# Optimization experiments

Hardware: AMD Instinct MI355X
Metric: run time of the kernel (lower is better)

Reference implementation:

```python
import jax, jax.numpy as jnp
import numpy as np

EPS = 1.0  # global `epsilon` in the original code
B, C, N, T = 4, 32, 256, 288
NUM_PRED, NUM_LOCAL = 12, 12
PERIOD, SHORT, LONG = 24, 12, 48
EMB = 16
RE_K = 5  # ResidualExtrapolate kernel width (num_input)


def const_extrap(x, p):
    # replicate-pad right by p along time
    return jnp.concatenate([x, jnp.repeat(x[..., -1:], p, axis=-1)], axis=-1)


def seasonal_extrap(x, p):
    # circular-pad right by p along time (p <= t)
    return jnp.concatenate([x, x[..., :p]], axis=-1)


def term_norm(x, L):
    # sliding-window mean/var over last axis, window L, replicate-padded left.
    pad1 = [(0, 0)] * 3 + [(1, 0)]
    cs = jnp.pad(jnp.cumsum(x, axis=-1), pad1)
    cs2 = jnp.pad(jnp.cumsum(x * x, axis=-1), pad1)
    mean = (cs[..., L:] - cs[..., :-L]) / L            # (b,c,n,t-L+1)
    var = (cs2[..., L:] - cs2[..., :-L]) / L - mean ** 2 + 1e-5
    padL = [(0, 0)] * 3 + [(L - 1, 0)]
    mean = jnp.pad(mean, padL, mode='edge')
    var = jnp.pad(var, padL, mode='edge')
    out = (x - mean) / jnp.sqrt(var + EPS)
    return out, mean, jnp.sqrt(var)


def seasonal_norm(x, P):
    b, c, n, t = x.shape
    xp = x.reshape(b, c, n, t // P, P)
    mean = xp.mean(3)                                   # (b,c,n,P) per-phase
    var = (xp ** 2).mean(3) - mean ** 2 + 1e-5
    mean = jnp.tile(mean, (1, 1, 1, t // P))
    var = jnp.tile(var, (1, 1, 1, t // P))
    out = (x - mean) / jnp.sqrt(var + EPS)
    return out, mean, jnp.sqrt(var)


def spatial_norm(x, emb):
    n = emb.shape[0]
    adj = emb @ emb.T - 10.0 * jnp.eye(n, dtype=x.dtype)
    adj = jax.nn.softmax(adj, axis=-1)                  # (n,n)
    mean = jnp.einsum('nm,bcmt->bcnt', adj, x)
    var = jnp.einsum('nm,bcmt->bcnt', adj, x * x) - mean ** 2 + 1e-5
    out = (x - mean) / jnp.sqrt(var + EPS)
    return out, mean, jnp.sqrt(var)


def residual_extrap(x, W, bias):
    # Conv2d(c -> c*num_pred, kernel (1, RE_K)) on last RE_K steps, then cat.
    b, c, n, t = x.shape
    y = jnp.einsum('ock,bcnk->bon', W[:, :, 0, :], x[..., -RE_K:]) + bias[None, :, None]
    proj = y.reshape(b, NUM_PRED, c, n).transpose(0, 2, 3, 1)  # (b,c,n,num_pred)
    return jnp.concatenate([x, proj], axis=-1)


def conv_time(x, W, bias):
    y = jax.lax.conv_general_dilated(x, W, (1, 1), 'VALID',
                                     dimension_numbers=('NCHW', 'OIHW', 'NCHW'))
    return y + bias[None, :, None, None]


def conv1x1(x, W, bias):
    return jnp.einsum('oc,bcnt->bont', W[:, :, 0, 0], x) + bias[None, :, None, None]


def setup_inputs() -> dict:
    key = jax.random.key(0)
    ks = jax.random.split(key, 16)
    f32 = jnp.float32

    def w(k, shape, fan_in):
        return jax.random.normal(k, shape, dtype=f32) / np.sqrt(fan_in)

    inp = {
        'x': jax.random.normal(ks[0], (B, C, N, T), dtype=f32),
        'node_embedding': 0.1 * jax.random.normal(ks[1], (N, EMB), dtype=f32),
        'conv1_w': w(ks[6], (C, 13 * C, 1, NUM_LOCAL), 13 * C * NUM_LOCAL),
        'conv1_b': jnp.zeros((C,), f32),
        'conv2_w': w(ks[7], (C, 13 * C, 1, NUM_LOCAL), 13 * C * NUM_LOCAL),
        'conv2_b': jnp.zeros((C,), f32),
        'skip_w': w(ks[8], (C, C, 1, 1), C),
        'skip_b': jnp.zeros((C,), f32),
        'res_w': w(ks[9], (C, C, 1, 1), C),
        'res_b': jnp.zeros((C,), f32),
    }
    for i in range(4):
        inp[f're{i + 1}_w'] = w(ks[2 + i], (C * NUM_PRED, C, 1, RE_K), C * RE_K)
        inp[f're{i + 1}_b'] = jnp.zeros((C * NUM_PRED,), f32)
    return inp


def reference(x, node_embedding, conv1_w, conv1_b, conv2_w, conv2_b,
              skip_w, skip_b, res_w, res_b,
              re1_w, re1_b, re2_w, re2_b, re3_w, re3_b, re4_w, re4_b):
    xs, aux = [], []

    x_proj = const_extrap(x, NUM_PRED)
    zeros = jnp.zeros_like(x_proj)
    xs.append(x_proj); aux.append(zeros)

    x1, lt_mean, lt_std = term_norm(x, LONG)
    xp = residual_extrap(x1, re1_w, re1_b)
    mp, sp = const_extrap(lt_mean, NUM_PRED), const_extrap(lt_std, NUM_PRED)
    xs += [xp, mp, sp]; aux += [zeros, mp, sp]

    x2, se_mean, se_std = seasonal_norm(x1, PERIOD)
    xp = residual_extrap(x2, re2_w, re2_b)
    mp, sp = seasonal_extrap(se_mean, NUM_PRED), seasonal_extrap(se_std, NUM_PRED)
    xs += [xp, mp, sp]; aux += [zeros, mp, sp]

    x3, st_mean, st_std = term_norm(x2, SHORT)
    xp = residual_extrap(x3, re3_w, re3_b)
    mp, sp = const_extrap(st_mean, NUM_PRED), const_extrap(st_std, NUM_PRED)
    xs += [xp, mp, sp]; aux += [zeros, mp, sp]

    x4, sn_mean, sn_std = spatial_norm(x3, node_embedding)
    xp = residual_extrap(x4, re4_w, re4_b)
    mp, sp = const_extrap(sn_mean, NUM_PRED), const_extrap(sn_std, NUM_PRED)
    xs += [xp, mp, sp]; aux += [zeros, mp, sp]

    pad1 = [(0, 0)] * 3 + [(1, 0)]
    x_cat = jnp.pad(jnp.concatenate(xs, axis=1), pad1)      # (b,13c,n,T+P+1)
    a_cat = jnp.pad(jnp.concatenate(aux, axis=1), pad1)

    g1 = conv_time(x_cat, conv1_w, conv1_b)
    g2 = conv_time(x_cat, conv2_w, conv2_b)
    a1 = conv_time(a_cat, conv1_w, conv1_b)
    a2 = conv_time(a_cat, conv2_w, conv2_b)

    prod = g1 * g2
    x_z = conv1x1(prod[..., :-NUM_PRED], res_w, res_b)
    s = conv1x1(prod[..., -NUM_PRED:], skip_w, skip_b)
    s_aux = conv1x1((a1 * a2)[..., -NUM_PRED:], skip_w, skip_b)
    return (x_z, s_aux, s)
```

## Files before the change

kernel.cpp:

```cpp
#include <hip/hip_runtime.h>

typedef unsigned short u16;
typedef __attribute__((ext_vector_type(8))) short short8v;
typedef __attribute__((ext_vector_type(4))) float f32x4;

#define PSTR 304L
#define OFF_SAUX 9109504L
#define OFF_S    9502720L
#define CHSTR (32L*256L*PSTR)

static __device__ __forceinline__ float bf2f(u16 u) {
  return __uint_as_float(((unsigned int)u) << 16);
}
static __device__ __forceinline__ u16 f2bf(float f) {
  unsigned int i = __float_as_uint(f);
  i += 0x7FFFu + ((i >> 16) & 1u);
  return (u16)(i >> 16);
}

static __device__ __forceinline__ void gload16(const void* g, void* l) {
  __builtin_amdgcn_global_load_lds(
      (const __attribute__((address_space(1))) unsigned int*)g,
      (__attribute__((address_space(3))) unsigned int*)l, 16, 0, 0);
}

static __device__ void adj_body(int row, const float* __restrict__ emb,
                                u16* __restrict__ adjb) {
  const int m = threadIdx.x;
  __shared__ float sred[8];
  float er[16];
#pragma unroll
  for (int e = 0; e < 16; ++e) er[e] = emb[row * 16 + e];
  float d = 0.f;
#pragma unroll
  for (int e = 0; e < 16; ++e) d += er[e] * emb[m * 16 + e];
  if (m == row) d -= 10.f;
  float v = d;
#pragma unroll
  for (int off = 32; off; off >>= 1) v = fmaxf(v, __shfl_xor(v, off, 64));
  const int wid = m >> 6, lane = m & 63;
  if (lane == 0) sred[wid] = v;
  __syncthreads();
  const float mx = fmaxf(fmaxf(sred[0], sred[1]), fmaxf(sred[2], sred[3]));
  const float p = expf(d - mx);
  v = p;
#pragma unroll
  for (int off = 32; off; off >>= 1) v += __shfl_xor(v, off, 64);
  if (lane == 0) sred[4 + wid] = v;
  __syncthreads();
  const float sum = sred[4] + sred[5] + sred[6] + sred[7];
  adjb[row * 256 + m] = f2bf(p / sum);
}

static __device__ void prepw_body(int bid, const float* __restrict__ c1w,
                                  const float* __restrict__ c2w,
                                  u16* __restrict__ wB) {
  const int idx = bid * 256 + threadIdx.x;
  const int kk = idx >> 11;
  const int rem = idx & 2047;
  const int j = rem >> 5, chp = rem & 31;
  const int pslot = chp >> 3, chlo = chp & 7;
  const int sl = pslot ^ ((j >> 1) & 3);
  const int ch = sl * 8 + chlo;
  const int g = kk / 12, k = kk - g * 12;
  const int cin = g * 32 + ch;
  const float* src = (j < 32) ? c1w : c2w;
  const int jj = j & 31;
  wB[idx] = f2bf(src[(jj * 416 + cin) * 12 + k]);
}

static __device__ __forceinline__ void wscan2(float& s1, float& s2, int lane) {
#pragma unroll
  for (int off = 1; off < 64; off <<= 1) {
    float a = __shfl_up(s1, off, 64);
    float b = __shfl_up(s2, off, 64);
    if (lane >= off) { s1 += a; s2 += b; }
  }
}

static __device__ void norm_body(int bid, const float* __restrict__ x,
                                 u16* __restrict__ xcat) {
  const int wid = threadIdx.x >> 6, lane = threadIdx.x & 63;
  const long row = (long)bid * 4 + wid;
  const int b = (int)(row >> 13);
  const int c = (int)((row >> 8) & 31);
  const int n = (int)(row & 255);
  const float* xr = x + row * 288;
  __shared__ float bufA[4][304], bufB[4][304], cs1[4][312], cs2[4][312], sst[4][80];
  float* bA = bufA[wid];
  float* bB = bufB[wid];
  float* p1 = cs1[wid];
  float* p2 = cs2[wid];
  float* psm = sst[wid];
  float* psi = sst[wid] + 24;
  float* psd = sst[wid] + 48;
  const long chb = (long)b * 416 * 256 + n;

  for (int j = 0; j < 5; ++j) { int t = j * 64 + lane; if (t < 288) bA[t] = xr[t]; }

  auto scanbuf = [&](float* src) {
    float ca = 0.f, cb = 0.f;
    if (lane == 0) { p1[0] = 0.f; p2[0] = 0.f; }
    for (int j = 0; j < 5; ++j) {
      int t = j * 64 + lane;
      float v = (t < 288) ? src[t] : 0.f;
      float s1 = v, s2 = v * v;
      wscan2(s1, s2, lane);
      if (t < 288) { p1[t + 1] = ca + s1; p2[t + 1] = cb + s2; }
      ca += __shfl(s1, 63, 64);
      cb += __shfl(s2, 63, 64);
    }
  };

  scanbuf(bA);
  for (int j = 0; j < 5; ++j) {
    int t = j * 64 + lane; if (t >= 288) continue;
    float S, Q;
    if (t >= 47) { S = p1[t + 1] - p1[t - 47]; Q = p2[t + 1] - p2[t - 47]; }
    else         { S = p1[48];                 Q = p2[48]; }
    float m = S * (1.f / 48.f);
    float var = Q * (1.f / 48.f) - m * m + 1e-5f;
    float sd = sqrtf(var);
    float iv = rsqrtf(var + 1.f);
    float xv = bA[t];
    float x1 = (xv - m) * iv;
    bB[t] = x1;
    xcat[(chb + (long)(c)      * 256) * PSTR + 1 + t] = f2bf(xv);
    xcat[(chb + (long)(32 + c) * 256) * PSTR + 1 + t] = f2bf(x1);
    xcat[(chb + (long)(64 + c) * 256) * PSTR + 1 + t] = f2bf(m);
    xcat[(chb + (long)(96 + c) * 256) * PSTR + 1 + t] = f2bf(sd);
  }
  {
    float S = p1[288] - p1[240], Q = p2[288] - p2[240];
    float m = S * (1.f / 48.f);
    float var = Q * (1.f / 48.f) - m * m + 1e-5f;
    float sd = sqrtf(var);
    if (lane < 12) {
      xcat[(chb + (long)(c)      * 256) * PSTR + 289 + lane] = f2bf(bA[287]);
      xcat[(chb + (long)(64 + c) * 256) * PSTR + 289 + lane] = f2bf(m);
      xcat[(chb + (long)(96 + c) * 256) * PSTR + 289 + lane] = f2bf(sd);
    }
    if (lane == 0) {
      xcat[(chb + (long)(c)      * 256) * PSTR] = 0;
      xcat[(chb + (long)(32 + c) * 256) * PSTR] = 0;
      xcat[(chb + (long)(64 + c) * 256) * PSTR] = 0;
      xcat[(chb + (long)(96 + c) * 256) * PSTR] = 0;
    }
  }
  if (lane < 24) {
    float S = 0.f, Q = 0.f;
#pragma unroll
    for (int i2 = 0; i2 < 12; ++i2) { float v = bB[lane + 24 * i2]; S += v; Q += v * v; }
    float m = S * (1.f / 12.f);
    float var = Q * (1.f / 12.f) - m * m + 1e-5f;
    psm[lane] = m; psi[lane] = rsqrtf(var + 1.f); psd[lane] = sqrtf(var);
  }
  for (int j = 0; j < 5; ++j) {
    int t = j * 64 + lane; if (t >= 288) continue;
    int ph = t % 24;
    float m = psm[ph];
    float x2v = (bB[t] - m) * psi[ph];
    bA[t] = x2v;
    xcat[(chb + (long)(128 + c) * 256) * PSTR + 1 + t] = f2bf(x2v);
    xcat[(chb + (long)(160 + c) * 256) * PSTR + 1 + t] = f2bf(m);
    xcat[(chb + (long)(192 + c) * 256) * PSTR + 1 + t] = f2bf(psd[ph]);
  }
  if (lane < 12) {
    xcat[(chb + (long)(160 + c) * 256) * PSTR + 289 + lane] = f2bf(psm[lane]);
    xcat[(chb + (long)(192 + c) * 256) * PSTR + 289 + lane] = f2bf(psd[lane]);
  }
  if (lane == 0) {
    xcat[(chb + (long)(128 + c) * 256) * PSTR] = 0;
    xcat[(chb + (long)(160 + c) * 256) * PSTR] = 0;
    xcat[(chb + (long)(192 + c) * 256) * PSTR] = 0;
  }
  scanbuf(bA);
  for (int j = 0; j < 5; ++j) {
    int t = j * 64 + lane; if (t >= 288) continue;
    float S, Q;
    if (t >= 11) { S = p1[t + 1] - p1[t - 11]; Q = p2[t + 1] - p2[t - 11]; }
    else         { S = p1[12];                 Q = p2[12]; }
    float m = S * (1.f / 12.f);
    float var = Q * (1.f / 12.f) - m * m + 1e-5f;
    float sd = sqrtf(var);
    float iv = rsqrtf(var + 1.f);
    float x3v = (bA[t] - m) * iv;
    xcat[(chb + (long)(224 + c) * 256) * PSTR + 1 + t] = f2bf(x3v);
    xcat[(chb + (long)(256 + c) * 256) * PSTR + 1 + t] = f2bf(m);
    xcat[(chb + (long)(288 + c) * 256) * PSTR + 1 + t] = f2bf(sd);
  }
  {
    float S = p1[288] - p1[276], Q = p2[288] - p2[276];
    float m = S * (1.f / 12.f);
    float var = Q * (1.f / 12.f) - m * m + 1e-5f;
    float sd = sqrtf(var);
    if (lane < 12) {
      xcat[(chb + (long)(256 + c) * 256) * PSTR + 289 + lane] = f2bf(m);
      xcat[(chb + (long)(288 + c) * 256) * PSTR + 289 + lane] = f2bf(sd);
    }
    if (lane == 0) {
      xcat[(chb + (long)(224 + c) * 256) * PSTR] = 0;
      xcat[(chb + (long)(256 + c) * 256) * PSTR] = 0;
      xcat[(chb + (long)(288 + c) * 256) * PSTR] = 0;
    }
  }
}

__global__ __launch_bounds__(256) void k_front(const float* __restrict__ x,
    const float* __restrict__ emb, const float* __restrict__ c1w,
    const float* __restrict__ c2w, u16* __restrict__ xcat,
    u16* __restrict__ adjb, u16* __restrict__ wB) {
  const int bid = blockIdx.x;
  if (bid < 8192)       norm_body(bid, x, xcat);
  else if (bid < 8448)  adj_body(bid - 8192, emb, adjb);
  else                  prepw_body(bid - 8448, c1w, c2w, wB);
}

static __device__ void re_body(long gid, u16* __restrict__ xcat,
                               const float* __restrict__ W,
                               const float* __restrict__ bias, int srcch) {
  const int o = (int)(gid % 384);
  const long bn = gid / 384;
  const int n = (int)(bn & 255);
  const int b = (int)(bn >> 8);
  const float* wr = W + o * 160;
  float acc = bias[o];
  for (int c = 0; c < 32; ++c) {
    const long rb = ((long)(b * 416 + srcch + c) * 256 + n) * PSTR + 284;
#pragma unroll
    for (int k = 0; k < 5; ++k) acc += wr[c * 5 + k] * bf2f(xcat[rb + k]);
  }
  const int cd = o & 31, p = o >> 5;
  xcat[((long)(b * 416 + srcch + cd) * 256 + n) * PSTR + 289 + p] = f2bf(acc);
}

__global__ __launch_bounds__(256) void k_re4(u16* __restrict__ xcat,
                                             const float* __restrict__ W,
                                             const float* __restrict__ bias) {
  re_body((long)blockIdx.x * 256 + threadIdx.x, xcat, W, bias, 320);
}

static __device__ void spatial_body(int sid, u16* __restrict__ xcat,
                                    const u16* __restrict__ adjb) {
  const int gx = sid % 20;
  const int slice = sid / 20;
  const int tcn = gx >> 2, ncb = gx & 3;
  const int b = slice >> 5, c = slice & 31;
  const int t0 = tcn * 64, n0 = ncb * 64;
  const int tid = threadIdx.x;
  const int wid = tid >> 6, lane = tid & 63;
  const int wm = wid >> 1, wn = wid & 1;
  const int l15 = lane & 15, lq = lane >> 4;
  __shared__ __align__(16) u16 BT[2][64 * 40];
  __shared__ __align__(16) u16 BT2[2][64 * 40];
  const f32x4 vz = {0.f, 0.f, 0.f, 0.f};
  f32x4 aM[2][2], aV[2][2];
#pragma unroll
  for (int i = 0; i < 2; ++i)
#pragma unroll
    for (int j = 0; j < 2; ++j) { aM[i][j] = vz; aV[i][j] = vz; }
  const long base7 = (long)(b * 416 + 224 + c) * 256;
  u16 rv[8];
#pragma unroll
  for (int r = 0; r < 8; ++r) {
    int idx = tid + r * 256; int ml = idx >> 6, s = idx & 63;
    rv[r] = xcat[(base7 + ml) * PSTR + 1 + t0 + s];
  }
#pragma unroll
  for (int r = 0; r < 8; ++r) {
    int idx = tid + r * 256; int ml = idx >> 6, s = idx & 63;
    float v = bf2f(rv[r]);
    BT[0][s * 40 + ml] = rv[r];
    BT2[0][s * 40 + ml] = f2bf(v * v);
  }
  __syncthreads();
  int cur = 0;
  for (int kk = 0; kk < 8; ++kk) {
    u16 rn[8];
    if (kk < 7) {
#pragma unroll
      for (int r = 0; r < 8; ++r) {
        int idx = tid + r * 256; int ml = idx >> 6, s = idx & 63;
        rn[r] = xcat[(base7 + (long)((kk + 1) * 32 + ml)) * PSTR + 1 + t0 + s];
      }
    }
    const short8v a0 = *(const short8v*)(adjb + (long)(n0 + wm * 32 + l15) * 256 + kk * 32 + lq * 8);
    const short8v a1 = *(const short8v*)(adjb + (long)(n0 + wm * 32 + 16 + l15) * 256 + kk * 32 + lq * 8);
    const u16* bt = BT[cur];
    const u16* bq = BT2[cur];
    const short8v b0 = *(const short8v*)(bt + (wn * 32 + l15) * 40 + lq * 8);
    const short8v b1 = *(const short8v*)(bt + (wn * 32 + 16 + l15) * 40 + lq * 8);
    const short8v q0 = *(const short8v*)(bq + (wn * 32 + l15) * 40 + lq * 8);
    const short8v q1 = *(const short8v*)(bq + (wn * 32 + 16 + l15) * 40 + lq * 8);
    aM[0][0] = __builtin_amdgcn_mfma_f32_16x16x32_bf16(a0, b0, aM[0][0], 0, 0, 0);
    aM[0][1] = __builtin_amdgcn_mfma_f32_16x16x32_bf16(a0, b1, aM[0][1], 0, 0, 0);
    aM[1][0] = __builtin_amdgcn_mfma_f32_16x16x32_bf16(a1, b0, aM[1][0], 0, 0, 0);
    aM[1][1] = __builtin_amdgcn_mfma_f32_16x16x32_bf16(a1, b1, aM[1][1], 0, 0, 0);
    aV[0][0] = __builtin_amdgcn_mfma_f32_16x16x32_bf16(a0, q0, aV[0][0], 0, 0, 0);
    aV[0][1] = __builtin_amdgcn_mfma_f32_16x16x32_bf16(a0, q1, aV[0][1], 0, 0, 0);
    aV[1][0] = __builtin_amdgcn_mfma_f32_16x16x32_bf16(a1, q0, aV[1][0], 0, 0, 0);
    aV[1][1] = __builtin_amdgcn_mfma_f32_16x16x32_bf16(a1, q1, aV[1][1], 0, 0, 0);
    __syncthreads();
    if (kk < 7) {
#pragma unroll
      for (int r = 0; r < 8; ++r) {
        int idx = tid + r * 256; int ml = idx >> 6, s = idx & 63;
        float v = bf2f(rn[r]);
        BT[cur ^ 1][s * 40 + ml] = rn[r];
        BT2[cur ^ 1][s * 40 + ml] = f2bf(v * v);
      }
    }
    __syncthreads();
    cur ^= 1;
  }
#pragma unroll
  for (int mf = 0; mf < 2; ++mf)
#pragma unroll
    for (int nf = 0; nf < 2; ++nf)
#pragma unroll
      for (int e = 0; e < 4; ++e) {
        const int i = wm * 32 + mf * 16 + lq * 4 + e;
        const int j = wn * 32 + nf * 16 + l15;
        const int nn = n0 + i, tt2 = t0 + j;
        if (tt2 < 288) {
          const float mean = aM[mf][nf][e], ex2 = aV[mf][nf][e];
          const float var = ex2 - mean * mean + 1e-5f;
          const float sd = sqrtf(var);
          const float iv = rsqrtf(var + 1.f);
          const float x3c = bf2f(xcat[(base7 + nn) * PSTR + 1 + tt2]);
          const float x4 = (x3c - mean) * iv;
          const long r10 = ((long)(b * 416 + 320 + c) * 256 + nn) * PSTR;
          const long r11 = ((long)(b * 416 + 352 + c) * 256 + nn) * PSTR;
          const long r12 = ((long)(b * 416 + 384 + c) * 256 + nn) * PSTR;
          xcat[r10 + 1 + tt2] = f2bf(x4);
          xcat[r11 + 1 + tt2] = f2bf(mean);
          xcat[r12 + 1 + tt2] = f2bf(sd);
          if (tt2 == 287) {
            for (int p = 0; p < 12; ++p) {
              xcat[r11 + 289 + p] = f2bf(mean);
              xcat[r12 + 289 + p] = f2bf(sd);
            }
          }
          if (tt2 == 0) { xcat[r10] = 0; xcat[r11] = 0; xcat[r12] = 0; }
        }
      }
}

__global__ __launch_bounds__(256) void k_mid(u16* __restrict__ xcat,
    const u16* __restrict__ adjb,
    const float* __restrict__ w1, const float* __restrict__ b1,
    const float* __restrict__ w2, const float* __restrict__ b2,
    const float* __restrict__ w3, const float* __restrict__ b3) {
  const int bid = blockIdx.x;
  if (bid < 2560) { spatial_body(bid, xcat, adjb); return; }
  const int sub = bid - 2560;
  const int which = sub / 1536;
  const long gid = (long)(sub - which * 1536) * 256 + threadIdx.x;
  if (which == 0)      re_body(gid, xcat, w1, b1, 32);
  else if (which == 1) re_body(gid, xcat, w2, b2, 128);
  else                 re_body(gid, xcat, w3, b3, 224);
}

template<int MT>
static __device__ void convG_body(int t0, int by,
    const u16* __restrict__ xcat, const u16* __restrict__ wB,
    const float* __restrict__ c1b, const float* __restrict__ c2b,
    const float* __restrict__ rsw, const float* __restrict__ rsb,
    const float* __restrict__ skw, const float* __restrict__ skb,
    float* __restrict__ out, unsigned char* smem) {
  const int b = by >> 6;
  const int tid = threadIdx.x;
  const int wid = tid >> 6, lane = tid & 63;
  const int n_abs = (by & 63) * 4 + wid;
  const int l15 = lane & 15, lq = lane >> 4;
  constexpr int NCH = (MT == 2) ? 9 : 5;
  constexpr int TKS = (MT == 2) ? 18 : 10;

  u16* Asm = (u16*)smem;
  u16* Bsm = (u16*)(smem + 46080);

  int sch[NCH], stk[NCH];
  const u16* baseR[NCH];
#pragma unroll
  for (int r = 0; r < NCH; ++r) {
    int cc = r * 64 + lane;
    int s = cc / TKS, tk = cc - s * TKS;
    sch[r] = s; stk[r] = tk;
    baseR[r] = xcat + ((long)(b * 416 + s) * 256 + n_abs) * PSTR + t0 + tk * 8;
  }
  u16* aw = Asm + wid * 5760;

#define AWRITE() { \
    _Pragma("unroll") \
    for (int r = 0; r < NCH; ++r) { \
      u16 pc[8]; *(uint4*)pc = aR[r]; \
      const int pcol = ((((sch[r] >> 3) ^ stk[r]) & 3) << 3) + (sch[r] & 7); \
      _Pragma("unroll") \
      for (int e = 0; e < 8; ++e) aw[(stk[r] * 8 + e) * 40 + pcol] = pc[e]; \
    } }

  uint4 aR[NCH];
#pragma unroll
  for (int r = 0; r < NCH; ++r) aR[r] = *(const uint4*)baseR[r];
  AWRITE();
#pragma unroll
  for (int r = 0; r < NCH; ++r) aR[r] = *(const uint4*)(baseR[r] + CHSTR);
  gload16(wB + 0 * 2048 + wid * 512 + lane * 8, Bsm + 0 + wid * 512);
  gload16(wB + 1 * 2048 + wid * 512 + lane * 8, Bsm + 2048 + wid * 512);
  __syncthreads();

  const f32x4 vz = {0.f, 0.f, 0.f, 0.f};
  f32x4 acc[4 * MT][4];
#pragma unroll
  for (int i = 0; i < 4 * MT; ++i)
#pragma unroll
    for (int j = 0; j < 4; ++j) acc[i][j] = vz;

  const u16* bwl = Bsm + l15 * 32 + ((lq ^ ((l15 >> 1) & 3)) << 3);

  int p = 0;
  for (int g = 0; g < 13; ++g) {
    for (int kp = 0; kp < 6; ++kp) {
      if (p < 77) {
        const long kkn = (long)(p + 1) * 2;
        const int bufn = ((p + 1) & 1) * 4096;
        gload16(wB + kkn * 2048 + wid * 512 + lane * 8, Bsm + bufn + wid * 512);
        gload16(wB + (kkn + 1) * 2048 + wid * 512 + lane * 8, Bsm + bufn + 2048 + wid * 512);
      }
      const int bufc = (p & 1) * 4096;
#pragma unroll
      for (int kh = 0; kh < 2; ++kh) {
        const int K = kp * 2 + kh;
        short8v af[4 * MT], bf[4];
#pragma unroll
        for (int f = 0; f < 4 * MT; ++f) {
          const int tt = K + f * 16 + l15;
          af[f] = *(const short8v*)(aw + tt * 40 + (((lq ^ (tt >> 3)) & 3) << 3));
        }
#pragma unroll
        for (int f = 0; f < 4; ++f)
          bf[f] = *(const short8v*)(bwl + bufc + kh * 2048 + f * 512);
#pragma unroll
        for (int i = 0; i < 4 * MT; ++i)
#pragma unroll
          for (int j = 0; j < 4; ++j)
            acc[i][j] = __builtin_amdgcn_mfma_f32_16x16x32_bf16(af[i], bf[j], acc[i][j], 0, 0, 0);
      }
      __syncthreads();
      ++p;
    }
    if (g < 12) {
      AWRITE();
      if (g < 11) {
#pragma unroll
        for (int r = 0; r < NCH; ++r) aR[r] = *(const uint4*)(baseR[r] + (long)(g + 2) * CHSTR);
      }
    }
  }
#undef AWRITE
  __syncthreads();

#pragma unroll
  for (int pass = 0; pass < MT; ++pass) {
    float* pw = (float*)smem + wid * 2112;
#pragma unroll
    for (int fi = 0; fi < 4; ++fi)
#pragma unroll
      for (int nf = 0; nf < 2; ++nf)
#pragma unroll
        for (int e = 0; e < 4; ++e) {
          const int trow = fi * 16 + lq * 4 + e;
          const int cch = nf * 16 + l15;
          const float g1 = acc[pass * 4 + fi][nf][e] + c1b[cch];
          const float g2 = acc[pass * 4 + fi][nf + 2][e] + c2b[cch];
          pw[trow * 33 + cch] = g1 * g2;
        }
    float pv[32];
    {
      const float* prow = pw + lane * 33;
#pragma unroll
      for (int c = 0; c < 32; ++c) pv[c] = prow[c];
    }
    const int t = t0 + pass * 64 + lane;
    if (t0 + pass * 64 + 63 < 278) {
      for (int o = 0; o < 32; ++o) {
        float s = rsb[o];
        const float* wr = rsw + o * 32;
#pragma unroll
        for (int c = 0; c < 32; ++c) s += wr[c] * pv[c];
        out[((long)(b * 32 + o) * 256 + n_abs) * 278 + t] = s;
      }
    } else {
      const bool isres = t < 278;
      const bool isskip = (t >= 278) && (t < 290);
      for (int o = 0; o < 32; ++o) {
        const float* wr = (isres ? rsw : skw) + o * 32;
        float s = (isres ? rsb : skb)[o];
#pragma unroll
        for (int c = 0; c < 32; ++c) s += wr[c] * pv[c];
        if (isres)       out[((long)(b * 32 + o) * 256 + n_abs) * 278 + t] = s;
        else if (isskip) out[OFF_S + ((long)(b * 32 + o) * 256 + n_abs) * 12 + (t - 278)] = s;
      }
    }
  }
}

__global__ __launch_bounds__(256, 2) void k_convG(
    const u16* __restrict__ xcat, const u16* __restrict__ wB,
    const float* __restrict__ c1b, const float* __restrict__ c2b,
    const float* __restrict__ rsw, const float* __restrict__ rsb,
    const float* __restrict__ skw, const float* __restrict__ skb,
    float* __restrict__ out) {
  __shared__ __align__(16) unsigned char smem[62464];
  if (blockIdx.x < 2)
    convG_body<2>(blockIdx.x * 128, blockIdx.y, xcat, wB, c1b, c2b, rsw, rsb, skw, skb, out, smem);
  else
    convG_body<1>(256, blockIdx.y, xcat, wB, c1b, c2b, rsw, rsb, skw, skb, out, smem);
}

__global__ __launch_bounds__(256) void k_convA(const u16* __restrict__ xcat,
    const u16* __restrict__ wB, const float* __restrict__ c1b,
    const float* __restrict__ c2b, const float* __restrict__ skw,
    const float* __restrict__ skb, float* __restrict__ out) {
  const int tid = threadIdx.x;
  const int wid = tid >> 6, lane = tid & 63;
  const int row = blockIdx.x;
  const int b = row >> 8, n = row & 255;
  const int l15 = lane & 15, lq = lane >> 4;
  __shared__ __align__(16) u16 ATa[4][2][36 * 40];
  __shared__ float apL[4][16 * 68];
  const int gtab[8] = {2, 3, 5, 6, 8, 9, 11, 12};
  const long bnbase = (long)b * 416 * 256 + n;

#pragma unroll
  for (int tau = 0; tau < 2; ++tau) {
    const int g = gtab[wid * 2 + tau];
    u16* at = ATa[wid][tau];
#pragma unroll
    for (int h = 0; h < 2; ++h) {
      const int c = lane + h * 64;
      const int ch = c >> 2, part = c & 3;
      const uint4 v = *(const uint4*)(xcat +
          (bnbase + (long)(g * 32 + ch) * 256) * PSTR + 272 + part * 8);
      u16 pc[8]; *(uint4*)pc = v;
#pragma unroll
      for (int e = 0; e < 8; ++e) at[(part * 8 + e) * 40 + ch] = pc[e];
    }
  }

  const f32x4 vz = {0.f, 0.f, 0.f, 0.f};
  f32x4 acc[4] = {vz, vz, vz, vz};
  const int bsw = (lq ^ ((l15 >> 1) & 3)) << 3;
#pragma unroll
  for (int tau = 0; tau < 2; ++tau) {
    const int g = gtab[wid * 2 + tau];
    const u16* at = ATa[wid][tau];
    for (int k = 0; k < 12; ++k) {
      const short8v af = *(const short8v*)(at + (l15 + k + 6) * 40 + lq * 8);
#pragma unroll
      for (int nf = 0; nf < 4; ++nf) {
        const short8v bf = *(const short8v*)(wB + (long)(g * 12 + k) * 2048 + (nf * 16 + l15) * 32 + bsw);
        acc[nf] = __builtin_amdgcn_mfma_f32_16x16x32_bf16(af, bf, acc[nf], 0, 0, 0);
      }
    }
  }
  float* ap = apL[wid];
#pragma unroll
  for (int nf = 0; nf < 4; ++nf)
#pragma unroll
    for (int e = 0; e < 4; ++e)
      ap[(lq * 4 + e) * 68 + nf * 16 + l15] = acc[nf][e];
  __syncthreads();
  for (int idx = tid; idx < 1024; idx += 256) {
    const int m = idx >> 6, j = idx & 63;
    apL[0][m * 68 + j] = apL[0][m * 68 + j] + apL[1][m * 68 + j]
                       + apL[2][m * 68 + j] + apL[3][m * 68 + j];
  }
  __syncthreads();
  for (int task = tid; task < 384; task += 256) {
    const int o = task & 31, tt = task >> 5;
    float s = skb[o];
#pragma unroll
    for (int c2 = 0; c2 < 32; ++c2)
      s += skw[o * 32 + c2] * (apL[0][tt * 68 + c2] + c1b[c2])
                            * (apL[0][tt * 68 + 32 + c2] + c2b[c2]);
    out[OFF_SAUX + ((long)(b * 32 + o) * 256 + n) * 12 + tt] = s;
  }
}

extern "C" void kernel_launch(void* const* d_in, const int* in_sizes, int n_in,
                              void* d_out, int out_size, void* d_ws, size_t ws_size,
                              hipStream_t stream) {
  const float* x   = (const float*)d_in[0];
  const float* emb = (const float*)d_in[1];
  const float* c1w = (const float*)d_in[2];
  const float* c1b = (const float*)d_in[3];
  const float* c2w = (const float*)d_in[4];
  const float* c2b = (const float*)d_in[5];
  const float* skw = (const float*)d_in[6];
  const float* skb = (const float*)d_in[7];
  const float* rsw = (const float*)d_in[8];
  const float* rsb = (const float*)d_in[9];
  float* out = (float*)d_out;

  u16* xcat = (u16*)d_ws;
  u16* wB   = xcat + (4L * 416 * 256 * 304 + 2048);
  u16* adjb = wB + 156L * 2048;

  k_front<<<dim3(9696), dim3(256), 0, stream>>>(x, emb, c1w, c2w, xcat, adjb, wB);
  k_mid<<<dim3(7168), dim3(256), 0, stream>>>(xcat, adjb,
      (const float*)d_in[10], (const float*)d_in[11],
      (const float*)d_in[12], (const float*)d_in[13],
      (const float*)d_in[14], (const float*)d_in[15]);
  k_re4<<<dim3(1536), dim3(256), 0, stream>>>(xcat, (const float*)d_in[16], (const float*)d_in[17]);
  k_convG<<<dim3(3, 256), dim3(256), 0, stream>>>(xcat, wB, c1b, c2b, rsw, rsb, skw, skb, out);
  k_convA<<<dim3(1024), dim3(256), 0, stream>>>(xcat, wB, c1b, c2b, skw, skb, out);
}
```

Measured before the change: 604.9 us.

## Load conv weights directly from global memory instead of LDS double-buffering

```diff
diff --git a/kernel.cpp b/kernel.cpp
--- a/kernel.cpp
+++ b/kernel.cpp
@@ -16,12 +16,6 @@
   unsigned int i = __float_as_uint(f);
   i += 0x7FFFu + ((i >> 16) & 1u);
   return (u16)(i >> 16);
-}
-
-static __device__ __forceinline__ void gload16(const void* g, void* l) {
-  __builtin_amdgcn_global_load_lds(
-      (const __attribute__((address_space(1))) unsigned int*)g,
-      (__attribute__((address_space(3))) unsigned int*)l, 16, 0, 0);
 }
 
 static __device__ void adj_body(int row, const float* __restrict__ emb,
@@ -377,7 +371,6 @@
   constexpr int TKS = (MT == 2) ? 18 : 10;
 
   u16* Asm = (u16*)smem;
-  u16* Bsm = (u16*)(smem + 46080);
 
   int sch[NCH], stk[NCH];
   const u16* baseR[NCH];
@@ -403,11 +396,6 @@
 #pragma unroll
   for (int r = 0; r < NCH; ++r) aR[r] = *(const uint4*)baseR[r];
   AWRITE();
-#pragma unroll
-  for (int r = 0; r < NCH; ++r) aR[r] = *(const uint4*)(baseR[r] + CHSTR);
-  gload16(wB + 0 * 2048 + wid * 512 + lane * 8, Bsm + 0 + wid * 512);
-  gload16(wB + 1 * 2048 + wid * 512 + lane * 8, Bsm + 2048 + wid * 512);
-  __syncthreads();
 
   const f32x4 vz = {0.f, 0.f, 0.f, 0.f};
   f32x4 acc[4 * MT][4];
@@ -416,45 +404,33 @@
 #pragma unroll
     for (int j = 0; j < 4; ++j) acc[i][j] = vz;
 
-  const u16* bwl = Bsm + l15 * 32 + ((lq ^ ((l15 >> 1) & 3)) << 3);
-
-  int p = 0;
+  const int bsw = (lq ^ ((l15 >> 1) & 3)) << 3;
+
   for (int g = 0; g < 13; ++g) {
-    for (int kp = 0; kp < 6; ++kp) {
-      if (p < 77) {
-        const long kkn = (long)(p + 1) * 2;
-        const int bufn = ((p + 1) & 1) * 4096;
-        gload16(wB + kkn * 2048 + wid * 512 + lane * 8, Bsm + bufn + wid * 512);
-        gload16(wB + (kkn + 1) * 2048 + wid * 512 + lane * 8, Bsm + bufn + 2048 + wid * 512);
-      }
-      const int bufc = (p & 1) * 4096;
-#pragma unroll
-      for (int kh = 0; kh < 2; ++kh) {
-        const int K = kp * 2 + kh;
-        short8v af[4 * MT], bf[4];
-#pragma unroll
-        for (int f = 0; f < 4 * MT; ++f) {
-          const int tt = K + f * 16 + l15;
-          af[f] = *(const short8v*)(aw + tt * 40 + (((lq ^ (tt >> 3)) & 3) << 3));
-        }
-#pragma unroll
-        for (int f = 0; f < 4; ++f)
-          bf[f] = *(const short8v*)(bwl + bufc + kh * 2048 + f * 512);
-#pragma unroll
-        for (int i = 0; i < 4 * MT; ++i)
-#pragma unroll
-          for (int j = 0; j < 4; ++j)
-            acc[i][j] = __builtin_amdgcn_mfma_f32_16x16x32_bf16(af[i], bf[j], acc[i][j], 0, 0, 0);
-      }
-      __syncthreads();
-      ++p;
+    const u16* wg = wB + (long)g * 12 * 2048 + bsw;
+#pragma unroll
+    for (int K = 0; K < 12; ++K) {
+      const u16* wk = wg + K * 2048;
+      short8v bf[4];
+#pragma unroll
+      for (int f = 0; f < 4; ++f)
+        bf[f] = *(const short8v*)(wk + (f * 16 + l15) * 32);
+      short8v af[4 * MT];
+#pragma unroll
+      for (int f = 0; f < 4 * MT; ++f) {
+        const int tt = K + f * 16 + l15;
+        af[f] = *(const short8v*)(aw + tt * 40 + (((lq ^ (tt >> 3)) & 3) << 3));
+      }
+#pragma unroll
+      for (int i = 0; i < 4 * MT; ++i)
+#pragma unroll
+        for (int j = 0; j < 4; ++j)
+          acc[i][j] = __builtin_amdgcn_mfma_f32_16x16x32_bf16(af[i], bf[j], acc[i][j], 0, 0, 0);
     }
     if (g < 12) {
+#pragma unroll
+      for (int r = 0; r < NCH; ++r) aR[r] = *(const uint4*)(baseR[r] + (long)(g + 1) * CHSTR);
       AWRITE();
-      if (g < 11) {
-#pragma unroll
-        for (int r = 0; r < NCH; ++r) aR[r] = *(const uint4*)(baseR[r] + (long)(g + 2) * CHSTR);
-      }
     }
   }
 #undef AWRITE
@@ -511,7 +487,7 @@
     const float* __restrict__ rsw, const float* __restrict__ rsb,
     const float* __restrict__ skw, const float* __restrict__ skb,
     float* __restrict__ out) {
-  __shared__ __align__(16) unsigned char smem[62464];
+  __shared__ __align__(16) unsigned char smem[46080];
   if (blockIdx.x < 2)
     convG_body<2>(blockIdx.x * 128, blockIdx.y, xcat, wB, c1b, c2b, rsw, rsb, skw, skb, out, smem);
   else
```

Measured after the change: 965.0 us. +59.5%, slower.
